# Kernel optimization log

Measured on AMD Instinct MI355X. Metric: run time of the kernel, lower is better.

Reference implementation:

```python
import jax, jax.numpy as jnp
import numpy as np
from jax import lax

B, T, CIN, COUT, FACTOR = 2, 2048, 512, 512, 2
KUP = FACTOR * 2          # transposed-conv kernel
PUP = FACTOR // 2         # transposed-conv padding
KR, PR = 7, 3             # refine conv kernel/padding
EPS = 1e-5


def _ste(x, q):
    # straight-through estimator: forward = q, backward = identity
    return x + lax.stop_gradient(q - x)


def act_quant(x):
    # BitNet b1.58 per-token int8 absmax quant; x is (B, C, L), quant over C
    scale = 127.0 / jnp.maximum(jnp.max(jnp.abs(x), axis=1, keepdims=True), 1e-5)
    q = jnp.clip(jnp.round(x * scale), -128, 127) / scale
    return _ste(x, q)


def weight_quant(w):
    # ternary {-1,0,1} * scale, scale = mean |w|
    scale = 1.0 / jnp.maximum(jnp.mean(jnp.abs(w)), 1e-5)
    q = jnp.clip(jnp.round(w * scale), -1, 1) / scale
    return _ste(w, q)


def bit_conv1d(x, w, b, pad):
    # x: (B,C,L), w: (Cout,Cin,K) torch layout
    y = lax.conv_general_dilated(
        act_quant(x), weight_quant(w), window_strides=(1,),
        padding=[(pad, pad)], dimension_numbers=('NCH', 'OIH', 'NCH'))
    return y + b[None, :, None]


def bit_conv_transpose1d(x, w, b, stride, pad):
    # x: (B,Cin,L), w: (Cin,Cout,K) torch ConvTranspose1d layout
    k = w.shape[2]
    y = lax.conv_general_dilated(
        act_quant(x), jnp.flip(weight_quant(w), 2), window_strides=(1,),
        padding=[(k - 1 - pad, k - 1 - pad)], lhs_dilation=(stride,),
        dimension_numbers=('NCH', 'IOH', 'NCH'))
    return y + b[None, :, None]


def setup_inputs() -> dict:
    key = jax.random.key(0)
    ks = jax.random.split(key, 7)
    s_up = 1.0 / np.sqrt(CIN * KUP)
    s_r = 1.0 / np.sqrt(COUT * KR)
    return {
        'x': jax.random.normal(ks[0], (B, T, CIN), jnp.float32),
        'w_up': jax.random.normal(ks[1], (CIN, COUT, KUP), jnp.float32) * s_up,
        'b_up': jnp.zeros((COUT,), jnp.float32),
        'w_r1': jax.random.normal(ks[2], (COUT, COUT, KR), jnp.float32) * s_r,
        'b_r1': jnp.zeros((COUT,), jnp.float32),
        'w_r2': jax.random.normal(ks[3], (COUT, COUT, KR), jnp.float32) * s_r,
        'b_r2': jnp.zeros((COUT,), jnp.float32),
        'ln_w': jnp.ones((COUT,), jnp.float32),
        'ln_b': jnp.zeros((COUT,), jnp.float32),
    }


def reference(x, w_up, b_up, w_r1, b_r1, w_r2, b_r2, ln_w, ln_b):
    h = jnp.swapaxes(x, 1, 2)                                  # (B,Cin,T)
    h = bit_conv_transpose1d(h, w_up, b_up, FACTOR, PUP)       # (B,Cout,factor*T)
    r = bit_conv1d(h, w_r1, b_r1, PR)
    r = jax.nn.silu(r)
    r = bit_conv1d(r, w_r2, b_r2, PR)
    h = h + r
    h = jnp.swapaxes(h, 1, 2)                                  # (B,L,Cout)
    mu = jnp.mean(h, axis=-1, keepdims=True)
    var = jnp.mean(jnp.square(h - mu), axis=-1, keepdims=True)
    return (h - mu) * lax.rsqrt(var + EPS) * ln_w + ln_b
```

## Files before the change

### kernel.cpp

```cpp
#include <hip/hip_runtime.h>
#include <hip/hip_bf16.h>
#include <cstdint>
#include <cstddef>


#define B_ 2
#define T_ 2048
#define L_ 4096
#define C_ 512

static constexpr int NUP = 512 * 512 * 4;
static constexpr int NR  = 512 * 512 * 7;

using v4i  = __attribute__((ext_vector_type(4))) int;

__device__ __forceinline__ void gl16(const void* g, void* l) {
  __builtin_amdgcn_global_load_lds((const __attribute__((address_space(1))) unsigned int*)g,
                                   (__attribute__((address_space(3))) unsigned int*)l,
                                   16, 0, 0);
}


__device__ inline float block_reduce_sum_256(float v) {
  #pragma unroll
  for (int off = 32; off > 0; off >>= 1) v += __shfl_down(v, off, 64);
  __shared__ float s[4];
  __syncthreads();
  if ((threadIdx.x & 63) == 0) s[threadIdx.x >> 6] = v;
  __syncthreads();
  return (s[0] + s[1]) + (s[2] + s[3]);
}

__global__ void abssum3_partial(const float* __restrict__ w0, const float* __restrict__ w1,
                                const float* __restrict__ w2, float* __restrict__ partial) {
  int y = blockIdx.y;
  const float* w = (y == 0) ? w0 : (y == 1) ? w1 : w2;
  int n = (y == 0) ? NUP : NR;
  int idx = blockIdx.x * 256 + threadIdx.x;
  float s = 0.f;
  for (int i = idx; i < n; i += gridDim.x * 256) s += fabsf(w[i]);
  s = block_reduce_sum_256(s);
  if (threadIdx.x == 0) partial[y * 256 + blockIdx.x] = s;
}

__global__ void abssum3_final(const float* __restrict__ partial, float* __restrict__ out) {
  int y = blockIdx.x;
  float v = partial[y * 256 + threadIdx.x];
  v = block_reduce_sum_256(v);
  if (threadIdx.x == 0) out[y] = v;
}

__global__ void tern_all_kernel(const float* __restrict__ wu, const float* __restrict__ w1,
                                const float* __restrict__ w2, int8_t* __restrict__ ou,
                                int8_t* __restrict__ o1, int8_t* __restrict__ o2,
                                const float* __restrict__ wsum) {
  int y = blockIdx.y;
  int idx = blockIdx.x * 256 + threadIdx.x;
  if (y == 0) {
    if (idx >= NUP) return;
    float mean = wsum[0] * (1.0f / (float)NUP);
    float scale = 1.0f / fmaxf(mean, 1e-5f);
    float t = rintf(wu[idx] * scale);
    t = fminf(fmaxf(t, -1.f), 1.f);
    int ci = idx >> 11;
    int co = (idx >> 2) & 511;
    int k = idx & 3;
    int ptap = (k == 3) ? 0 : (k == 1) ? 1 : (k == 2) ? 2 : 3;
    ou[(((size_t)ptap * 32 + (ci >> 4)) * 512 + co) * 16 + (ci & 15)] = (int8_t)t;
  } else {
    if (idx >= NR) return;
    const float* w = (y == 1) ? w1 : w2;
    int8_t* o = (y == 1) ? o1 : o2;
    float mean = wsum[y] * (1.0f / (float)NR);
    float scale = 1.0f / fmaxf(mean, 1e-5f);
    float t = rintf(w[idx] * scale);
    t = fminf(fmaxf(t, -1.f), 1.f);
    int co = idx / 3584;
    int rem = idx - co * 3584;
    int ci = rem / 7;
    int k = rem - ci * 7;
    o[(((size_t)k * 32 + (ci >> 4)) * 512 + co) * 16 + (ci & 15)] = (int8_t)t;
  }
}

__global__ void act_quant_kernel(const float* __restrict__ x, int8_t* __restrict__ qd,
                                 float* __restrict__ inv, int Lb, int lbsh, int LinH) {
  int tok = blockIdx.x;
  int b = tok >> lbsh;
  int t = tok & (Lb - 1);
  const float* row = x + (size_t)tok * C_;
  int tid = threadIdx.x;
  float v0 = row[tid];
  float v1 = row[tid + 256];
  float m = fmaxf(fabsf(v0), fabsf(v1));
  #pragma unroll
  for (int off = 32; off > 0; off >>= 1) m = fmaxf(m, __shfl_down(m, off, 64));
  __shared__ float s[4];
  __shared__ __align__(16) int8_t sq[512];
  if ((tid & 63) == 0) s[tid >> 6] = m;
  __syncthreads();
  m = fmaxf(fmaxf(s[0], s[1]), fmaxf(s[2], s[3]));
  float scale = 127.0f / fmaxf(m, 1e-5f);
  float q0 = fminf(fmaxf(rintf(v0 * scale), -128.f), 127.f);
  float q1 = fminf(fmaxf(rintf(v1 * scale), -128.f), 127.f);
  sq[tid] = (int8_t)q0;
  sq[tid + 256] = (int8_t)q1;
  __syncthreads();
  if (tid < 32)
    *(v4i*)(qd + ((size_t)(b * 32 + tid) * LinH + 8 + t) * 16) = *(const v4i*)(sq + tid * 16);
  if (tid == 0) inv[(size_t)b * LinH + 8 + t] = 1.0f / scale;
}

template<int NTAPS, bool CONVT, int EPI>
__global__ __launch_bounds__(1024, 8)
void conv_fused(const int8_t* __restrict__ qin, const float* __restrict__ invp, int LinH,
                const int8_t* __restrict__ wq, const float* __restrict__ wsum, int widx,
                float wninv, const float* __restrict__ bias,
                float* __restrict__ hout,
                int8_t* __restrict__ qout, float* __restrict__ invout, int LoutH,
                const float* __restrict__ res, const float* __restrict__ g,
                const float* __restrict__ be, float* __restrict__ lnout, int Lout) {
  __shared__ __align__(16) int8_t sA[32 * 22 * 16];
  __shared__ float sInv[24];
  __shared__ float sRedA[16][16];
  __shared__ float sRedB[16][16];
  __shared__ float sS0[16];
  __shared__ float sS1[16];
  __shared__ __align__(16) int8_t sQ[16][512];

  const int tid = threadIdx.x;
  const int w = tid >> 6, lane = tid & 63;
  const int l15 = lane & 15, l4 = lane >> 4;
  const int t0 = blockIdx.x * 16;
  const int b = blockIdx.y;
  int s0 = -3;
  const int8_t* wq_p = wq;
  int parity = 0;
  if (CONVT) {
    parity = blockIdx.z;
    s0 = parity - 1;
    wq_p += (size_t)parity * 2 * 32 * 512 * 16;
  }
  const int8_t* qin_b = qin + (size_t)b * 32 * LinH * 16;
  const float* inv_b = invp + (size_t)b * LinH + 8;

  {
    int base = w * 64;
    if (base < 704) {
      int u = base + lane;
      int kq = u / 22;
      int row = u - kq * 22;
      gl16(qin_b + ((size_t)kq * LinH + (size_t)(t0 + 5 + row)) * 16,
           sA + (size_t)base * 16);
    }
  }
  if (tid < 22) sInv[tid] = inv_b[t0 - 3 + tid];
  __syncthreads();

  float fs0[4], fs1[4];
  v4i acc0{}, acc1{};
  #pragma unroll
  for (int r = 0; r < 4; ++r) { fs0[r] = 0.f; fs1[r] = 0.f; acc0[r] = 0; acc1[r] = 0; }

  const int c0 = w * 32;
  const int8_t* wb = wq_p + ((size_t)l4 * 512 + (size_t)(c0 + l15)) * 16;
  const int8_t* aB = sA + (size_t)l4 * (22 * 16);

  #pragma unroll 1
  for (int tap = 0; tap < NTAPS; ++tap) {
    const int shift = s0 + tap;
    const int8_t* aP = aB + (size_t)(3 + shift + l15) * 16;
    const int8_t* wt = wb + (size_t)tap * (32 * 512 * 16);
    #pragma unroll
    for (int kc = 0; kc < 8; ++kc) {
      v4i a  = *(const v4i*)(aP + (size_t)kc * (4 * 22 * 16));
      v4i b0 = *(const v4i*)(wt + (size_t)kc * 32768);
      v4i b1 = *(const v4i*)(wt + (size_t)kc * 32768 + 256);
      acc0 = __builtin_amdgcn_mfma_i32_16x16x64_i8(a, b0, acc0, 0, 0, 0);
      acc1 = __builtin_amdgcn_mfma_i32_16x16x64_i8(a, b1, acc1, 0, 0, 0);
    }
    #pragma unroll
    for (int r = 0; r < 4; ++r) {
      float sc = sInv[3 + shift + l4 * 4 + r];
      fs0[r] = fmaf((float)acc0[r], sc, fs0[r]);
      fs1[r] = fmaf((float)acc1[r], sc, fs1[r]);
      acc0[r] = 0; acc1[r] = 0;
    }
  }

  const float wdq = fmaxf(wsum[widx] * wninv, 1e-5f);
  const float bv0 = bias[c0 + l15];
  const float bv1 = bias[c0 + 16 + l15];
  #pragma unroll
  for (int r = 0; r < 4; ++r) {
    fs0[r] = fs0[r] * wdq + bv0;
    fs1[r] = fs1[r] * wdq + bv1;
  }

  if constexpr (EPI == 0) {
    #pragma unroll
    for (int r = 0; r < 4; ++r) {
      int m = l4 * 4 + r;
      size_t base = ((size_t)b * Lout + 2 * (size_t)(t0 + m) + parity) * 512;
      hout[base + c0 + l15] = fs0[r];
      hout[base + c0 + 16 + l15] = fs1[r];
    }
  }
  if constexpr (EPI == 1) {
    #pragma unroll
    for (int r = 0; r < 4; ++r) {
      fs0[r] = fs0[r] / (1.0f + expf(-fs0[r]));
      fs1[r] = fs1[r] / (1.0f + expf(-fs1[r]));
    }
  }

  if constexpr (EPI <= 1) {
    #pragma unroll
    for (int r = 0; r < 4; ++r) {
      int m = l4 * 4 + r;
      float mv = fmaxf(fabsf(fs0[r]), fabsf(fs1[r]));
      #pragma unroll
      for (int off = 8; off > 0; off >>= 1) mv = fmaxf(mv, __shfl_xor(mv, off, 64));
      if (l15 == 0) sRedA[w][m] = mv;
    }
    __syncthreads();
    if (tid < 16) {
      float mval = sRedA[0][tid];
      #pragma unroll
      for (int ww = 1; ww < 16; ++ww) mval = fmaxf(mval, sRedA[ww][tid]);
      float mm = fmaxf(mval, 1e-5f);
      sS0[tid] = 127.0f / mm;
      int tok = CONVT ? (2 * (t0 + tid) + parity) : (t0 + tid);
      invout[(size_t)b * LoutH + 8 + tok] = mm * (1.0f / 127.0f);
    }
    __syncthreads();
    #pragma unroll
    for (int r = 0; r < 4; ++r) {
      int m = l4 * 4 + r;
      float sc = sS0[m];
      float q0 = fminf(fmaxf(rintf(fs0[r] * sc), -128.f), 127.f);
      float q1 = fminf(fmaxf(rintf(fs1[r] * sc), -128.f), 127.f);
      sQ[m][c0 + l15] = (int8_t)q0;
      sQ[m][c0 + 16 + l15] = (int8_t)q1;
    }
    __syncthreads();
    if (tid < 512) {
      int row = tid >> 5, unit = tid & 31;
      int tok = CONVT ? (2 * (t0 + row) + parity) : (t0 + row);
      *(v4i*)(qout + (((size_t)b * 32 + unit) * LoutH + 8 + tok) * 16) =
          *(const v4i*)(&sQ[row][unit * 16]);
    }
  } else {
    #pragma unroll
    for (int r = 0; r < 4; ++r) {
      int m = l4 * 4 + r;
      size_t base = ((size_t)b * Lout + (size_t)(t0 + m)) * 512;
      fs0[r] += res[base + c0 + l15];
      fs1[r] += res[base + c0 + 16 + l15];
    }
    #pragma unroll
    for (int r = 0; r < 4; ++r) {
      int m = l4 * 4 + r;
      float s = fs0[r] + fs1[r];
      #pragma unroll
      for (int off = 8; off > 0; off >>= 1) s += __shfl_xor(s, off, 64);
      if (l15 == 0) sRedA[w][m] = s;
    }
    __syncthreads();
    if (tid < 16) {
      float s = sRedA[0][tid];
      #pragma unroll
      for (int ww = 1; ww < 16; ++ww) s += sRedA[ww][tid];
      sS0[tid] = s * (1.0f / 512.0f);
    }
    __syncthreads();
    #pragma unroll
    for (int r = 0; r < 4; ++r) {
      int m = l4 * 4 + r;
      float mu = sS0[m];
      float d0 = fs0[r] - mu, d1 = fs1[r] - mu;
      float ss = d0 * d0 + d1 * d1;
      #pragma unroll
      for (int off = 8; off > 0; off >>= 1) ss += __shfl_xor(ss, off, 64);
      if (l15 == 0) sRedB[w][m] = ss;
    }
    __syncthreads();
    if (tid < 16) {
      float ssum = sRedB[0][tid];
      #pragma unroll
      for (int ww = 1; ww < 16; ++ww) ssum += sRedB[ww][tid];
      float var = ssum * (1.0f / 512.0f);
      sS1[tid] = 1.0f / sqrtf(var + 1e-5f);
    }
    __syncthreads();
    const float g0 = g[c0 + l15], g1 = g[c0 + 16 + l15];
    const float e0 = be[c0 + l15], e1 = be[c0 + 16 + l15];
    #pragma unroll
    for (int r = 0; r < 4; ++r) {
      int m = l4 * 4 + r;
      float mu = sS0[m], rs = sS1[m];
      size_t base = ((size_t)b * Lout + (size_t)(t0 + m)) * 512;
      lnout[base + c0 + l15]      = (fs0[r] - mu) * rs * g0 + e0;
      lnout[base + c0 + 16 + l15] = (fs1[r] - mu) * rs * g1 + e1;
    }
  }
}


extern "C" void kernel_launch(void* const* d_in, const int* in_sizes, int n_in,
                              void* d_out, int out_size, void* d_ws, size_t ws_size,
                              hipStream_t stream) {
  const float* x    = (const float*)d_in[0];
  const float* w_up = (const float*)d_in[1];
  const float* b_up = (const float*)d_in[2];
  const float* w_r1 = (const float*)d_in[3];
  const float* b_r1 = (const float*)d_in[4];
  const float* w_r2 = (const float*)d_in[5];
  const float* b_r2 = (const float*)d_in[6];
  const float* ln_w = (const float*)d_in[7];
  const float* ln_b = (const float*)d_in[8];
  float* out = (float*)d_out;

  const int LXH = T_ + 16;
  const int LHH = L_ + 16;

  char* ws = (char*)d_ws;
  size_t off = 0;
  auto alloc = [&](size_t sz) { size_t p = off; off += (sz + 255) & ~(size_t)255; return p; };
  float*  wsum  = (float*) (ws + alloc(256));
  int8_t* qx    = (int8_t*)(ws + alloc((size_t)B_ * 32 * LXH * 16));
  int8_t* qh    = (int8_t*)(ws + alloc((size_t)B_ * 32 * LHH * 16));
  int8_t* qh2   = (int8_t*)(ws + alloc((size_t)B_ * 32 * LHH * 16));
  float*  invx  = (float*) (ws + alloc((size_t)B_ * LXH * 4));
  float*  invh  = (float*) (ws + alloc((size_t)B_ * LHH * 4));
  float*  invh2 = (float*) (ws + alloc((size_t)B_ * LHH * 4));
  size_t zero_bytes = off;
  float*  partial = (float*)(ws + alloc(3 * 256 * 4));
  int8_t* wqup = (int8_t*)(ws + alloc((size_t)4 * 32 * 512 * 16));
  int8_t* wq1  = (int8_t*)(ws + alloc((size_t)7 * 32 * 512 * 16));
  int8_t* wq2  = (int8_t*)(ws + alloc((size_t)7 * 32 * 512 * 16));
  float*  h    = (float*) (ws + alloc((size_t)B_ * L_ * C_ * 4));

  hipMemsetAsync(ws, 0, zero_bytes, stream);

  abssum3_partial<<<dim3(256, 3), 256, 0, stream>>>(w_up, w_r1, w_r2, partial);
  abssum3_final<<<3, 256, 0, stream>>>(partial, wsum);
  tern_all_kernel<<<dim3(NR / 256, 3), 256, 0, stream>>>(w_up, w_r1, w_r2,
                                                         wqup, wq1, wq2, wsum);

  act_quant_kernel<<<B_ * T_, 256, 0, stream>>>(x, qx, invx, T_, 11, LXH);

  conv_fused<2, true, 0><<<dim3(T_ / 16, B_, 2), 1024, 0, stream>>>(
      qx, invx, LXH, wqup, wsum, 0, 1.0f / (float)NUP, b_up,
      h, qh, invh, LHH, nullptr, nullptr, nullptr, nullptr, L_);

  conv_fused<7, false, 1><<<dim3(L_ / 16, B_, 1), 1024, 0, stream>>>(
      qh, invh, LHH, wq1, wsum, 1, 1.0f / (float)NR, b_r1,
      nullptr, qh2, invh2, LHH, nullptr, nullptr, nullptr, nullptr, L_);

  conv_fused<7, false, 2><<<dim3(L_ / 16, B_, 1), 1024, 0, stream>>>(
      qh2, invh2, LHH, wq2, wsum, 2, 1.0f / (float)NR, b_r2,
      nullptr, nullptr, nullptr, 0, h, ln_w, ln_b, out, L_);
}
```

Baseline: 214.8 us.

## Double token tile per block to reuse weight fragments across two MFMA row tiles

Each conv block now covers 32 tokens instead of 16, and every wave issues four MFMAs per k-chunk so each global weight load feeds two activation row tiles. This halves the number of blocks and the weight traffic per token, which matters because the weights are read from global memory in every block. In exchange each thread holds twice as many accumulators, the launch bound drops to 4 waves-per-EU, and there are half as many blocks (256 per conv) to spread across CUs.

```diff
diff --git a/kernel.cpp b/kernel.cpp
--- a/kernel.cpp
+++ b/kernel.cpp
@@ -112,7 +112,7 @@
 }
 
 template<int NTAPS, bool CONVT, int EPI>
-__global__ __launch_bounds__(1024, 8)
+__global__ __launch_bounds__(1024, 4)
 void conv_fused(const int8_t* __restrict__ qin, const float* __restrict__ invp, int LinH,
                 const int8_t* __restrict__ wq, const float* __restrict__ wsum, int widx,
                 float wninv, const float* __restrict__ bias,
@@ -120,18 +120,18 @@
                 int8_t* __restrict__ qout, float* __restrict__ invout, int LoutH,
                 const float* __restrict__ res, const float* __restrict__ g,
                 const float* __restrict__ be, float* __restrict__ lnout, int Lout) {
-  __shared__ __align__(16) int8_t sA[32 * 22 * 16];
-  __shared__ float sInv[24];
-  __shared__ float sRedA[16][16];
-  __shared__ float sRedB[16][16];
-  __shared__ float sS0[16];
-  __shared__ float sS1[16];
-  __shared__ __align__(16) int8_t sQ[16][512];
+  __shared__ __align__(16) int8_t sA[32 * 38 * 16];
+  __shared__ float sInv[40];
+  __shared__ float sRedA[16][32];
+  __shared__ float sRedB[16][32];
+  __shared__ float sS0[32];
+  __shared__ float sS1[32];
+  __shared__ __align__(16) int8_t sQ[32][512];
 
   const int tid = threadIdx.x;
   const int w = tid >> 6, lane = tid & 63;
   const int l15 = lane & 15, l4 = lane >> 4;
-  const int t0 = blockIdx.x * 16;
+  const int t0 = blockIdx.x * 32;
   const int b = blockIdx.y;
   int s0 = -3;
   const int8_t* wq_p = wq;
@@ -144,27 +144,31 @@
   const int8_t* qin_b = qin + (size_t)b * 32 * LinH * 16;
   const float* inv_b = invp + (size_t)b * LinH + 8;
 
-  {
-    int base = w * 64;
-    if (base < 704) {
+  #pragma unroll
+  for (int i = 0; i < 2; ++i) {
+    int base = i * 1024 + w * 64;
+    if (base < 1216) {
       int u = base + lane;
-      int kq = u / 22;
-      int row = u - kq * 22;
+      int kq = u / 38;
+      int row = u - kq * 38;
       gl16(qin_b + ((size_t)kq * LinH + (size_t)(t0 + 5 + row)) * 16,
            sA + (size_t)base * 16);
     }
   }
-  if (tid < 22) sInv[tid] = inv_b[t0 - 3 + tid];
+  if (tid < 38) sInv[tid] = inv_b[t0 - 3 + tid];
   __syncthreads();
 
-  float fs0[4], fs1[4];
-  v4i acc0{}, acc1{};
+  float fs00[4], fs01[4], fs10[4], fs11[4];
+  v4i acc00{}, acc01{}, acc10{}, acc11{};
   #pragma unroll
-  for (int r = 0; r < 4; ++r) { fs0[r] = 0.f; fs1[r] = 0.f; acc0[r] = 0; acc1[r] = 0; }
+  for (int r = 0; r < 4; ++r) {
+    fs00[r] = 0.f; fs01[r] = 0.f; fs10[r] = 0.f; fs11[r] = 0.f;
+    acc00[r] = 0; acc01[r] = 0; acc10[r] = 0; acc11[r] = 0;
+  }
 
   const int c0 = w * 32;
   const int8_t* wb = wq_p + ((size_t)l4 * 512 + (size_t)(c0 + l15)) * 16;
-  const int8_t* aB = sA + (size_t)l4 * (22 * 16);
+  const int8_t* aB = sA + (size_t)l4 * (38 * 16);
 
   #pragma unroll 1
   for (int tap = 0; tap < NTAPS; ++tap) {
@@ -173,18 +177,24 @@
     const int8_t* wt = wb + (size_t)tap * (32 * 512 * 16);
     #pragma unroll
     for (int kc = 0; kc < 8; ++kc) {
-      v4i a  = *(const v4i*)(aP + (size_t)kc * (4 * 22 * 16));
+      v4i a0 = *(const v4i*)(aP + (size_t)kc * (4 * 38 * 16));
+      v4i a1 = *(const v4i*)(aP + (size_t)kc * (4 * 38 * 16) + 256);
       v4i b0 = *(const v4i*)(wt + (size_t)kc * 32768);
       v4i b1 = *(const v4i*)(wt + (size_t)kc * 32768 + 256);
-      acc0 = __builtin_amdgcn_mfma_i32_16x16x64_i8(a, b0, acc0, 0, 0, 0);
-      acc1 = __builtin_amdgcn_mfma_i32_16x16x64_i8(a, b1, acc1, 0, 0, 0);
+      acc00 = __builtin_amdgcn_mfma_i32_16x16x64_i8(a0, b0, acc00, 0, 0, 0);
+      acc01 = __builtin_amdgcn_mfma_i32_16x16x64_i8(a0, b1, acc01, 0, 0, 0);
+      acc10 = __builtin_amdgcn_mfma_i32_16x16x64_i8(a1, b0, acc10, 0, 0, 0);
+      acc11 = __builtin_amdgcn_mfma_i32_16x16x64_i8(a1, b1, acc11, 0, 0, 0);
     }
     #pragma unroll
     for (int r = 0; r < 4; ++r) {
-      float sc = sInv[3 + shift + l4 * 4 + r];
-      fs0[r] = fmaf((float)acc0[r], sc, fs0[r]);
-      fs1[r] = fmaf((float)acc1[r], sc, fs1[r]);
-      acc0[r] = 0; acc1[r] = 0;
+      float sc0 = sInv[3 + shift + l4 * 4 + r];
+      float sc1 = sInv[3 + shift + 16 + l4 * 4 + r];
+      fs00[r] = fmaf((float)acc00[r], sc0, fs00[r]);
+      fs01[r] = fmaf((float)acc01[r], sc0, fs01[r]);
+      fs10[r] = fmaf((float)acc10[r], sc1, fs10[r]);
+      fs11[r] = fmaf((float)acc11[r], sc1, fs11[r]);
+      acc00[r] = 0; acc01[r] = 0; acc10[r] = 0; acc11[r] = 0;
     }
   }
 
@@ -193,38 +203,49 @@
   const float bv1 = bias[c0 + 16 + l15];
   #pragma unroll
   for (int r = 0; r < 4; ++r) {
-    fs0[r] = fs0[r] * wdq + bv0;
-    fs1[r] = fs1[r] * wdq + bv1;
+    fs00[r] = fs00[r] * wdq + bv0;
+    fs01[r] = fs01[r] * wdq + bv1;
+    fs10[r] = fs10[r] * wdq + bv0;
+    fs11[r] = fs11[r] * wdq + bv1;
   }
 
   if constexpr (EPI == 0) {
     #pragma unroll
+    for (int mrep = 0; mrep < 2; ++mrep) {
+      #pragma unroll
+      for (int r = 0; r < 4; ++r) {
+        int m = mrep * 16 + l4 * 4 + r;
+        size_t base = ((size_t)b * Lout + 2 * (size_t)(t0 + m) + parity) * 512;
+        hout[base + c0 + l15]      = (mrep == 0) ? fs00[r] : fs10[r];
+        hout[base + c0 + 16 + l15] = (mrep == 0) ? fs01[r] : fs11[r];
+      }
+    }
+  }
+  if constexpr (EPI == 1) {
+    #pragma unroll
     for (int r = 0; r < 4; ++r) {
-      int m = l4 * 4 + r;
-      size_t base = ((size_t)b * Lout + 2 * (size_t)(t0 + m) + parity) * 512;
-      hout[base + c0 + l15] = fs0[r];
-      hout[base + c0 + 16 + l15] = fs1[r];
-    }
-  }
-  if constexpr (EPI == 1) {
-    #pragma unroll
-    for (int r = 0; r < 4; ++r) {
-      fs0[r] = fs0[r] / (1.0f + expf(-fs0[r]));
-      fs1[r] = fs1[r] / (1.0f + expf(-fs1[r]));
+      fs00[r] = fs00[r] / (1.0f + expf(-fs00[r]));
+      fs01[r] = fs01[r] / (1.0f + expf(-fs01[r]));
+      fs10[r] = fs10[r] / (1.0f + expf(-fs10[r]));
+      fs11[r] = fs11[r] / (1.0f + expf(-fs11[r]));
     }
   }
 
   if constexpr (EPI <= 1) {
     #pragma unroll
-    for (int r = 0; r < 4; ++r) {
-      int m = l4 * 4 + r;
-      float mv = fmaxf(fabsf(fs0[r]), fabsf(fs1[r]));
-      #pragma unroll
-      for (int off = 8; off > 0; off >>= 1) mv = fmaxf(mv, __shfl_xor(mv, off, 64));
-      if (l15 == 0) sRedA[w][m] = mv;
-    }
-    __syncthreads();
-    if (tid < 16) {
+    for (int mrep = 0; mrep < 2; ++mrep) {
+      #pragma unroll
+      for (int r = 0; r < 4; ++r) {
+        int m = mrep * 16 + l4 * 4 + r;
+        float mv = (mrep == 0) ? fmaxf(fabsf(fs00[r]), fabsf(fs01[r]))
+                               : fmaxf(fabsf(fs10[r]), fabsf(fs11[r]));
+        #pragma unroll
+        for (int off = 8; off > 0; off >>= 1) mv = fmaxf(mv, __shfl_xor(mv, off, 64));
+        if (l15 == 0) sRedA[w][m] = mv;
+      }
+    }
+    __syncthreads();
+    if (tid < 32) {
       float mval = sRedA[0][tid];
       #pragma unroll
       for (int ww = 1; ww < 16; ++ww) mval = fmaxf(mval, sRedA[ww][tid]);
@@ -235,16 +256,21 @@
     }
     __syncthreads();
     #pragma unroll
-    for (int r = 0; r < 4; ++r) {
-      int m = l4 * 4 + r;
-      float sc = sS0[m];
-      float q0 = fminf(fmaxf(rintf(fs0[r] * sc), -128.f), 127.f);
-      float q1 = fminf(fmaxf(rintf(fs1[r] * sc), -128.f), 127.f);
-      sQ[m][c0 + l15] = (int8_t)q0;
-      sQ[m][c0 + 16 + l15] = (int8_t)q1;
-    }
-    __syncthreads();
-    if (tid < 512) {
+    for (int mrep = 0; mrep < 2; ++mrep) {
+      #pragma unroll
+      for (int r = 0; r < 4; ++r) {
+        int m = mrep * 16 + l4 * 4 + r;
+        float sc = sS0[m];
+        float v0 = (mrep == 0) ? fs00[r] : fs10[r];
+        float v1 = (mrep == 0) ? fs01[r] : fs11[r];
+        float q0 = fminf(fmaxf(rintf(v0 * sc), -128.f), 127.f);
+        float q1 = fminf(fmaxf(rintf(v1 * sc), -128.f), 127.f);
+        sQ[m][c0 + l15] = (int8_t)q0;
+        sQ[m][c0 + 16 + l15] = (int8_t)q1;
+      }
+    }
+    __syncthreads();
+    {
       int row = tid >> 5, unit = tid & 31;
       int tok = CONVT ? (2 * (t0 + row) + parity) : (t0 + row);
       *(v4i*)(qout + (((size_t)b * 32 + unit) * LoutH + 8 + tok) * 16) =
@@ -252,22 +278,28 @@
     }
   } else {
     #pragma unroll
-    for (int r = 0; r < 4; ++r) {
-      int m = l4 * 4 + r;
-      size_t base = ((size_t)b * Lout + (size_t)(t0 + m)) * 512;
-      fs0[r] += res[base + c0 + l15];
-      fs1[r] += res[base + c0 + 16 + l15];
-    }
-    #pragma unroll
-    for (int r = 0; r < 4; ++r) {
-      int m = l4 * 4 + r;
-      float s = fs0[r] + fs1[r];
-      #pragma unroll
-      for (int off = 8; off > 0; off >>= 1) s += __shfl_xor(s, off, 64);
-      if (l15 == 0) sRedA[w][m] = s;
-    }
-    __syncthreads();
-    if (tid < 16) {
+    for (int mrep = 0; mrep < 2; ++mrep) {
+      #pragma unroll
+      for (int r = 0; r < 4; ++r) {
+        int m = mrep * 16 + l4 * 4 + r;
+        size_t base = ((size_t)b * Lout + (size_t)(t0 + m)) * 512;
+        if (mrep == 0) { fs00[r] += res[base + c0 + l15]; fs01[r] += res[base + c0 + 16 + l15]; }
+        else           { fs10[r] += res[base + c0 + l15]; fs11[r] += res[base + c0 + 16 + l15]; }
+      }
+    }
+    #pragma unroll
+    for (int mrep = 0; mrep < 2; ++mrep) {
+      #pragma unroll
+      for (int r = 0; r < 4; ++r) {
+        int m = mrep * 16 + l4 * 4 + r;
+        float s = (mrep == 0) ? (fs00[r] + fs01[r]) : (fs10[r] + fs11[r]);
+        #pragma unroll
+        for (int off = 8; off > 0; off >>= 1) s += __shfl_xor(s, off, 64);
+        if (l15 == 0) sRedA[w][m] = s;
+      }
+    }
+    __syncthreads();
+    if (tid < 32) {
       float s = sRedA[0][tid];
       #pragma unroll
       for (int ww = 1; ww < 16; ++ww) s += sRedA[ww][tid];
@@ -275,17 +307,21 @@
     }
     __syncthreads();
     #pragma unroll
-    for (int r = 0; r < 4; ++r) {
-      int m = l4 * 4 + r;
-      float mu = sS0[m];
-      float d0 = fs0[r] - mu, d1 = fs1[r] - mu;
-      float ss = d0 * d0 + d1 * d1;
-      #pragma unroll
-      for (int off = 8; off > 0; off >>= 1) ss += __shfl_xor(ss, off, 64);
-      if (l15 == 0) sRedB[w][m] = ss;
-    }
-    __syncthreads();
-    if (tid < 16) {
+    for (int mrep = 0; mrep < 2; ++mrep) {
+      #pragma unroll
+      for (int r = 0; r < 4; ++r) {
+        int m = mrep * 16 + l4 * 4 + r;
+        float mu = sS0[m];
+        float d0 = ((mrep == 0) ? fs00[r] : fs10[r]) - mu;
+        float d1 = ((mrep == 0) ? fs01[r] : fs11[r]) - mu;
+        float ss = d0 * d0 + d1 * d1;
+        #pragma unroll
+        for (int off = 8; off > 0; off >>= 1) ss += __shfl_xor(ss, off, 64);
+        if (l15 == 0) sRedB[w][m] = ss;
+      }
+    }
+    __syncthreads();
+    if (tid < 32) {
       float ssum = sRedB[0][tid];
       #pragma unroll
       for (int ww = 1; ww < 16; ++ww) ssum += sRedB[ww][tid];
@@ -296,12 +332,17 @@
     const float g0 = g[c0 + l15], g1 = g[c0 + 16 + l15];
     const float e0 = be[c0 + l15], e1 = be[c0 + 16 + l15];
     #pragma unroll
-    for (int r = 0; r < 4; ++r) {
-      int m = l4 * 4 + r;
-      float mu = sS0[m], rs = sS1[m];
-      size_t base = ((size_t)b * Lout + (size_t)(t0 + m)) * 512;
-      lnout[base + c0 + l15]      = (fs0[r] - mu) * rs * g0 + e0;
-      lnout[base + c0 + 16 + l15] = (fs1[r] - mu) * rs * g1 + e1;
+    for (int mrep = 0; mrep < 2; ++mrep) {
+      #pragma unroll
+      for (int r = 0; r < 4; ++r) {
+        int m = mrep * 16 + l4 * 4 + r;
+        float mu = sS0[m], rs = sS1[m];
+        size_t base = ((size_t)b * Lout + (size_t)(t0 + m)) * 512;
+        float v0 = (mrep == 0) ? fs00[r] : fs10[r];
+        float v1 = (mrep == 0) ? fs01[r] : fs11[r];
+        lnout[base + c0 + l15]      = (v0 - mu) * rs * g0 + e0;
+        lnout[base + c0 + 16 + l15] = (v1 - mu) * rs * g1 + e1;
+      }
     }
   }
 }
@@ -350,15 +391,15 @@
 
   act_quant_kernel<<<B_ * T_, 256, 0, stream>>>(x, qx, invx, T_, 11, LXH);
 
-  conv_fused<2, true, 0><<<dim3(T_ / 16, B_, 2), 1024, 0, stream>>>(
+  conv_fused<2, true, 0><<<dim3(T_ / 32, B_, 2), 1024, 0, stream>>>(
       qx, invx, LXH, wqup, wsum, 0, 1.0f / (float)NUP, b_up,
       h, qh, invh, LHH, nullptr, nullptr, nullptr, nullptr, L_);
 
-  conv_fused<7, false, 1><<<dim3(L_ / 16, B_, 1), 1024, 0, stream>>>(
+  conv_fused<7, false, 1><<<dim3(L_ / 32, B_, 1), 1024, 0, stream>>>(
       qh, invh, LHH, wq1, wsum, 1, 1.0f / (float)NR, b_r1,
       nullptr, qh2, invh2, LHH, nullptr, nullptr, nullptr, nullptr, L_);
 
-  conv_fused<7, false, 2><<<dim3(L_ / 16, B_, 1), 1024, 0, stream>>>(
+  conv_fused<7, false, 2><<<dim3(L_ / 32, B_, 1), 1024, 0, stream>>>(
       qh2, invh2, LHH, wq2, wsum, 2, 1.0f / (float)NR, b_r2,
       nullptr, nullptr, nullptr, 0, h, ln_w, ln_b, out, L_);
 }
```

New measurement: 184.9 us, median of 2. -13.9%, faster.
